# Optimization experiments

Hardware: AMD Instinct MI355X
Metric: run time of the kernel (lower is better)

The kernel has to match this reference:

```python
import jax, jax.numpy as jnp
import numpy as np

IN_DIM = 256
DIM_MSA = 32
PAIR_DIM = 64
B, L = 1, 1024


def setup_inputs() -> dict:
    key = jax.random.key(0)
    ks = jax.random.split(key, 6)
    seq_rep = jax.random.normal(ks[0], (B, L, IN_DIM), dtype=jnp.float32)
    pair_rep = jax.random.normal(ks[1], (B, L, L, PAIR_DIM), dtype=jnp.float32)
    # nn.Linear params: W [out, in], b [out]
    W1 = jax.random.normal(ks[2], (DIM_MSA, IN_DIM), dtype=jnp.float32) * (1.0 / np.sqrt(IN_DIM))
    b1 = jax.random.normal(ks[3], (DIM_MSA,), dtype=jnp.float32) * 0.01
    W2 = jax.random.normal(ks[4], (PAIR_DIM, DIM_MSA * DIM_MSA), dtype=jnp.float32) * (1.0 / np.sqrt(DIM_MSA * DIM_MSA))
    b2 = jax.random.normal(ks[5], (PAIR_DIM,), dtype=jnp.float32) * 0.01
    return {"seq_rep": seq_rep, "pair_rep": pair_rep, "W1": W1, "b1": b1, "W2": W2, "b2": b2}


def reference(seq_rep, pair_rep, W1, b1, W2, b2):
    # proj_down1: [B,L,in_dim] -> [B,L,c] where c = dim_msa
    s = seq_rep @ W1.T + b1  # [B,L,c]
    # Original: outer[b,i,j,c,d] = s[b,i,d] * s[b,j,c]; flatten (c d); proj_down2.
    # Reassociated (same math, no B*L*L*c*d intermediate):
    # out[b,i,j,p] = sum_{c,d} W2[p, c*DIM_MSA + d] * s[b,j,c] * s[b,i,d]
    Wp = W2.reshape(PAIR_DIM, DIM_MSA, DIM_MSA)  # [p, c, d]
    tmp = jnp.einsum('bjc,pcd->bjpd', s, Wp)      # [B,L,p,d]
    out = jnp.einsum('bid,bjpd->bijp', s, tmp) + b2  # [B,L,L,p]
    out = out + pair_rep
    return out
```

## Files before the change

### kernel.cpp

```cpp
#include <hip/hip_runtime.h>
#include <hip/hip_bf16.h>

#define L_SEQ    1024
#define IN_DIM   256
#define DIM_MSA  32
#define PAIR_DIM 64

typedef float f4 __attribute__((ext_vector_type(4)));
typedef short s8 __attribute__((ext_vector_type(8)));

__device__ __forceinline__ unsigned short f2bf(float f) {
    unsigned u = __float_as_uint(f);
    u = (u + 0x7FFFu + ((u >> 16) & 1u)) >> 16;
    return (unsigned short)u;
}

__global__ void k_proj1(const float* __restrict__ seq, const float* __restrict__ W1,
                        const float* __restrict__ b1, float* __restrict__ s,
                        unsigned short* __restrict__ s_bf) {
    int t = blockIdx.x * blockDim.x + threadIdx.x;
    int i = t >> 5, c = t & 31;
    const float4* sq = (const float4*)(seq + i * IN_DIM);
    const float4* w  = (const float4*)(W1  + c * IN_DIM);
    float a0 = 0.f, a1 = 0.f, a2 = 0.f, a3 = 0.f;
#pragma unroll
    for (int d4 = 0; d4 < IN_DIM / 4; ++d4) {
        float4 x = sq[d4], y = w[d4];
        a0 += x.x * y.x;  a1 += x.y * y.y;
        a2 += x.z * y.z;  a3 += x.w * y.w;
    }
    float v = b1[c] + ((a0 + a1) + (a2 + a3));
    s[t]    = v;
    s_bf[t] = f2bf(v);
}

__global__ void k_proj2(const float* __restrict__ s, const float* __restrict__ W2,
                        unsigned short* __restrict__ tmp_bf) {
    int t = blockIdx.x * blockDim.x + threadIdx.x;
    int q = t & 7, p = (t >> 3) & 63, j = t >> 9;
    const float4* w  = (const float4*)W2;
    const float*  sj = s + j * DIM_MSA;
    float4 acc = {0.f, 0.f, 0.f, 0.f};
#pragma unroll
    for (int c = 0; c < DIM_MSA; ++c) {
        float  sc = sj[c];
        float4 wv = w[p * 256 + c * 8 + q];
        acc.x += sc * wv.x;  acc.y += sc * wv.y;
        acc.z += sc * wv.z;  acc.w += sc * wv.w;
    }
    ushort4 o;
    o.x = f2bf(acc.x);  o.y = f2bf(acc.y);
    o.z = f2bf(acc.z);  o.w = f2bf(acc.w);
    ((ushort4*)tmp_bf)[t] = o;
}

__global__ __launch_bounds__(256) void k_outer_mfma5(
    const unsigned short* __restrict__ s_bf, const unsigned short* __restrict__ tmp_bf,
    const float* __restrict__ pair, const float* __restrict__ b2,
    float* __restrict__ out) {
    __shared__ float lds[4 * 16 * 256];
    int tid = threadIdx.x;
    int w = tid >> 6, l = tid & 63;
    int n = l & 15, kg = l >> 4;
    int jb = blockIdx.x & 63;
    int it = blockIdx.x >> 6;

    s8 a = *(const s8*)(s_bf + (size_t)(it * 16 + n) * DIM_MSA + kg * 8);

    int jp0 = jb * 1024 + w * 256;
    const unsigned short* bp = tmp_bf + (size_t)(jp0 + n) * DIM_MSA + kg * 8;
    float* myl = lds + w * 4096;

#pragma unroll
    for (int t = 0; t < 16; ++t) {
        s8 b = *(const s8*)(bp + (size_t)t * 16 * DIM_MSA);
        f4 z = {0.f, 0.f, 0.f, 0.f};
        f4 c = __builtin_amdgcn_mfma_f32_16x16x32_bf16(a, b, z, 0, 0, 0);
        float* dst = myl + (kg * 4) * 256 + t * 16 + n;
        dst[0]   = c.x;
        dst[256] = c.y;
        dst[512] = c.z;
        dst[768] = c.w;
    }

    f4 b4 = *(const f4*)(b2 + ((l * 4) & 63));
    size_t rowbase = (size_t)(it * 16) * 65536 + (size_t)jp0 + l * 4;
    const float* pp = pair + rowbase;
    float*       op = out  + rowbase;

#pragma unroll
    for (int i = 0; i < 16; ++i) {
        f4 cc = *(const f4*)(myl + i * 256 + l * 4);
        f4 pv = *(const f4*)(pp + (size_t)i * 65536);
        *(f4*)(op + (size_t)i * 65536) = cc + b4 + pv;
    }
}

extern "C" void kernel_launch(void* const* d_in, const int* in_sizes, int n_in,
                              void* d_out, int out_size, void* d_ws, size_t ws_size,
                              hipStream_t stream) {
    const float* seq  = (const float*)d_in[0];
    const float* pair = (const float*)d_in[1];
    const float* W1   = (const float*)d_in[2];
    const float* b1   = (const float*)d_in[3];
    const float* W2   = (const float*)d_in[4];
    const float* b2   = (const float*)d_in[5];
    float* out = (float*)d_out;

    float*          s_ws = (float*)d_ws;
    unsigned short* sbf  = (unsigned short*)(s_ws + 32768);
    unsigned short* tbf  = sbf + 32768;

    k_proj1<<<(L_SEQ * DIM_MSA) / 256, 256, 0, stream>>>(seq, W1, b1, s_ws, sbf);
    k_proj2<<<(L_SEQ * PAIR_DIM * (DIM_MSA / 4)) / 256, 256, 0, stream>>>(s_ws, W2, tbf);
    k_outer_mfma5<<<64 * 64, 256, 0, stream>>>(sbf, tbf, pair, b2, out);
}
```

Measured before the change: 129.5 us.

## Process two column tiles per block, prefetch B operands, use nontemporal stores

Each block now handles two j-tiles instead of one, so the grid is halved. The second tile's tmp_bf operands are loaded into registers while the first tile's epilogue streams pair/out. Output stores become nontemporal to avoid polluting cache, and launch bounds request two blocks per CU. The register array of 16 s8 values raises register pressure, and the LDS buffer is reused between the two tiles within each wave.

```diff
diff --git a/kernel.cpp b/kernel.cpp
--- a/kernel.cpp
+++ b/kernel.cpp
@@ -54,7 +54,7 @@
     ((ushort4*)tmp_bf)[t] = o;
 }
 
-__global__ __launch_bounds__(256) void k_outer_mfma5(
+__global__ __launch_bounds__(256, 2) void k_outer_mfma7(
     const unsigned short* __restrict__ s_bf, const unsigned short* __restrict__ tmp_bf,
     const float* __restrict__ pair, const float* __restrict__ b2,
     float* __restrict__ out) {
@@ -62,37 +62,68 @@
     int tid = threadIdx.x;
     int w = tid >> 6, l = tid & 63;
     int n = l & 15, kg = l >> 4;
-    int jb = blockIdx.x & 63;
-    int it = blockIdx.x >> 6;
+    int jb0 = blockIdx.x & 31;
+    int it  = blockIdx.x >> 5;
+    int jb1 = jb0 + 32;
 
     s8 a = *(const s8*)(s_bf + (size_t)(it * 16 + n) * DIM_MSA + kg * 8);
+    float* myl = lds + w * 4096;
+    f4 b4 = *(const f4*)(b2 + ((l * 4) & 63));
 
-    int jp0 = jb * 1024 + w * 256;
-    const unsigned short* bp = tmp_bf + (size_t)(jp0 + n) * DIM_MSA + kg * 8;
-    float* myl = lds + w * 4096;
+    int jp0 = jb0 * 1024 + w * 256;
+    int jp1 = jb1 * 1024 + w * 256;
+    const unsigned short* bp0 = tmp_bf + (size_t)(jp0 + n) * DIM_MSA + kg * 8;
+    const unsigned short* bp1 = tmp_bf + (size_t)(jp1 + n) * DIM_MSA + kg * 8;
+    size_t rb0 = (size_t)(it * 16) * 65536 + (size_t)jp0 + l * 4;
+    size_t rb1 = (size_t)(it * 16) * 65536 + (size_t)jp1 + l * 4;
 
+    s8 b[16];
+#pragma unroll
+    for (int t = 0; t < 16; ++t)
+        b[t] = *(const s8*)(bp0 + (size_t)t * 512);
 #pragma unroll
     for (int t = 0; t < 16; ++t) {
-        s8 b = *(const s8*)(bp + (size_t)t * 16 * DIM_MSA);
         f4 z = {0.f, 0.f, 0.f, 0.f};
-        f4 c = __builtin_amdgcn_mfma_f32_16x16x32_bf16(a, b, z, 0, 0, 0);
+        f4 c = __builtin_amdgcn_mfma_f32_16x16x32_bf16(a, b[t], z, 0, 0, 0);
         float* dst = myl + (kg * 4) * 256 + t * 16 + n;
         dst[0]   = c.x;
         dst[256] = c.y;
         dst[512] = c.z;
         dst[768] = c.w;
     }
+#pragma unroll
+    for (int t = 0; t < 16; ++t)
+        b[t] = *(const s8*)(bp1 + (size_t)t * 512);
 
-    f4 b4 = *(const f4*)(b2 + ((l * 4) & 63));
-    size_t rowbase = (size_t)(it * 16) * 65536 + (size_t)jp0 + l * 4;
-    const float* pp = pair + rowbase;
-    float*       op = out  + rowbase;
-
+    {
+        const float* pp = pair + rb0;
+        float*       op = out  + rb0;
 #pragma unroll
-    for (int i = 0; i < 16; ++i) {
-        f4 cc = *(const f4*)(myl + i * 256 + l * 4);
-        f4 pv = *(const f4*)(pp + (size_t)i * 65536);
-        *(f4*)(op + (size_t)i * 65536) = cc + b4 + pv;
+        for (int i = 0; i < 16; ++i) {
+            f4 cc = *(const f4*)(myl + i * 256 + l * 4);
+            f4 pv = *(const f4*)(pp + (size_t)i * 65536);
+            __builtin_nontemporal_store(cc + b4 + pv, (f4*)(op + (size_t)i * 65536));
+        }
+    }
+#pragma unroll
+    for (int t = 0; t < 16; ++t) {
+        f4 z = {0.f, 0.f, 0.f, 0.f};
+        f4 c = __builtin_amdgcn_mfma_f32_16x16x32_bf16(a, b[t], z, 0, 0, 0);
+        float* dst = myl + (kg * 4) * 256 + t * 16 + n;
+        dst[0]   = c.x;
+        dst[256] = c.y;
+        dst[512] = c.z;
+        dst[768] = c.w;
+    }
+    {
+        const float* pp = pair + rb1;
+        float*       op = out  + rb1;
+#pragma unroll
+        for (int i = 0; i < 16; ++i) {
+            f4 cc = *(const f4*)(myl + i * 256 + l * 4);
+            f4 pv = *(const f4*)(pp + (size_t)i * 65536);
+            __builtin_nontemporal_store(cc + b4 + pv, (f4*)(op + (size_t)i * 65536));
+        }
     }
 }
 
@@ -113,5 +144,5 @@
 
     k_proj1<<<(L_SEQ * DIM_MSA) / 256, 256, 0, stream>>>(seq, W1, b1, s_ws, sbf);
     k_proj2<<<(L_SEQ * PAIR_DIM * (DIM_MSA / 4)) / 256, 256, 0, stream>>>(s_ws, W2, tbf);
-    k_outer_mfma5<<<64 * 64, 256, 0, stream>>>(sbf, tbf, pair, b2, out);
+    k_outer_mfma7<<<64 * 32, 256, 0, stream>>>(sbf, tbf, pair, b2, out);
 }
```

After: 121.2 us. 1.07x faster.
